# Kernel tuning notes

Measured on AMD Instinct MI355X. Metric: run time of the kernel, lower is better.

## Reference

```python
import jax, jax.numpy as jnp
import numpy as np
from jax import lax

LENGTH, WIDTH = 64, 64
INPUT_DIM = 1


def _convlstm_layer(x_tbchw, W, b):
    """Run one ConvLSTM layer over time. x_tbchw: (L,B,Cin,H,W).
    W: (4*hid, Cin+hid, 3, 3), b: (4*hid,). Returns (outputs (L,B,hid,H,W), last_h)."""
    L, B, _, H, Wd = x_tbchw.shape
    hid = W.shape[0] // 4
    h0 = jnp.zeros((B, hid, H, Wd), dtype=x_tbchw.dtype)
    c0 = jnp.zeros((B, hid, H, Wd), dtype=x_tbchw.dtype)

    def step(carry, xt):
        h, c = carry
        z = lax.conv_general_dilated(
            jnp.concatenate([xt, h], axis=1), W,
            window_strides=(1, 1), padding='SAME',
            dimension_numbers=('NCHW', 'OIHW', 'NCHW'))
        z = z + b[None, :, None, None]
        cc_i, cc_f, cc_o, cc_g = jnp.split(z, 4, axis=1)
        c_next = jax.nn.sigmoid(cc_f) * c + jax.nn.sigmoid(cc_i) * jnp.tanh(cc_g)
        h_next = jax.nn.sigmoid(cc_o) * jnp.tanh(c_next)
        return (h_next, c_next), h_next

    (h_last, _), outs = lax.scan(step, (h0, c0), x_tbchw)
    return outs, h_last


def setup_inputs() -> dict:
    key = jax.random.key(0)
    k1, k2, k3 = jax.random.split(key, 3)
    B, L, N = 16, 12, LENGTH * WIDTH
    emd, out_len = 128, 12
    return {
        'history_data': jax.random.normal(k1, (B, L, N, 1), dtype=jnp.float32),
        'future_data': jnp.zeros((B, L, N, 1), dtype=jnp.float32),
        'W0': jax.random.normal(k2, (4 * emd, INPUT_DIM + emd, 3, 3), dtype=jnp.float32) * 0.05,
        'b0': jnp.zeros((4 * emd,), dtype=jnp.float32),
        'W1': jax.random.normal(k3, (4 * out_len, emd + out_len, 3, 3), dtype=jnp.float32) * 0.05,
        'b1': jnp.zeros((4 * out_len,), dtype=jnp.float32),
        'batch_seen': 0,
        'epoch': 0,
        'train': 1,
    }


def reference(history_data, future_data, W0, b0, W1, b1, batch_seen, epoch, train):
    B, L, N, C = history_data.shape
    # (B,L,1,H,W) -> (L,B,1,H,W) for time-major scan
    x = history_data[..., :INPUT_DIM].reshape(B, L, INPUT_DIM, LENGTH, WIDTH)
    x = jnp.transpose(x, (1, 0, 2, 3, 4))
    outs0, _ = _convlstm_layer(x, W0, b0)          # (L,B,emd,H,W)
    _, h_last = _convlstm_layer(outs0, W1, b1)     # (B,out_len,H,W)
    prediction = h_last.reshape(B, L, LENGTH * WIDTH)[..., None]  # (B,L,N,1)
    return prediction
```

## Files before the change

kernel.cpp:

```cpp
#include <hip/hip_runtime.h>
#include <hip/hip_bf16.h>


typedef __attribute__((ext_vector_type(8))) short short8;
typedef __attribute__((ext_vector_type(4))) float float4v;

#define CS 160
#define KTOT 1440
#define RSTR 2560
#define BSTR 10240
#define BSTR6 15360

__device__ __forceinline__ float sigf(float x) { return 1.f / (1.f + __expf(-x)); }
__device__ __forceinline__ short f2hs(float v) {
  _Float16 h = (_Float16)v;
  return *(short*)&h;
}
__device__ __forceinline__ float bs2f(short s) {
  __hip_bfloat16 h; *(short*)&h = s; return __bfloat162float(h);
}
__device__ __forceinline__ short f2bs(float v) {
  __hip_bfloat16 h = __float2bfloat16(v);
  return *(short*)&h;
}

__device__ __forceinline__ void async_ld16(const short* g, short* l) {
  __builtin_amdgcn_global_load_lds(
      (const __attribute__((address_space(1))) unsigned int*)g,
      (__attribute__((address_space(3))) unsigned int*)l, 16, 0, 0);
}

__device__ __forceinline__ void stage_one(const short* __restrict__ rowPtr, bool rowOK,
                                          short* dstRow, int lane,
                                          const short* __restrict__ zp, int j) {
  int e = j * 64 + lane;
  int px = e >> 2, v = e & 3;
  int xx = px - 1;
  bool ok = rowOK && (px < 66) && (xx >= 0) && (xx < 64);
  const short* g = ok ? (rowPtr + (size_t)xx * CS + v * 8) : zp;
  async_ld16(g, dstRow + e * 8);
}

__device__ __forceinline__ void stage_row(const short* __restrict__ rowPtr, bool rowOK,
                                          short* dstRow, int lane,
                                          const short* __restrict__ zp) {
  #pragma unroll
  for (int j = 0; j < 5; ++j) stage_one(rowPtr, rowOK, dstRow, lane, zp, j);
}

__global__ void detect_dtype(const unsigned short* __restrict__ w0, int* __restrict__ flag) {
  int lane = threadIdx.x;
  int cnt = 0;
  for (int i = 0; i < 4; ++i) {
    unsigned short u = w0[2 * (lane + 64 * i)];
    int e = (u >> 7) & 0xFF;
    unsigned long long b = __ballot(e >= 0xC0);
    cnt += __popcll(b);
  }
  if (lane == 0) *flag = (cnt > 32) ? 1 : 0;
}

__global__ void canon_x(const void* __restrict__ hist, short* __restrict__ Xc,
                        const int* __restrict__ flag) {
  int i = blockIdx.x * 256 + threadIdx.x;
  float v = (*flag) ? ((const float*)hist)[i] : bs2f(((const short*)hist)[i]);
  if (!isfinite(v) || fabsf(v) > 1e4f) v = 0.f;
  Xc[i] = f2hs(v);
}

__global__ void canon_b(const void* __restrict__ b0, const void* __restrict__ b1,
                        float* __restrict__ Bc0, float* __restrict__ Bc1,
                        const int* __restrict__ flag) {
  int i = blockIdx.x * 256 + threadIdx.x;
  int fl = *flag;
  if (i < 512) {
    float v = fl ? ((const float*)b0)[i] : bs2f(((const short*)b0)[i]);
    if (!isfinite(v) || fabsf(v) > 1e4f) v = 0.f;
    Bc0[i] = v;
  } else if (i < 560) {
    int j = i - 512;
    float v = fl ? ((const float*)b1)[j] : bs2f(((const short*)b1)[j]);
    if (!isfinite(v) || fabsf(v) > 1e4f) v = 0.f;
    Bc1[j] = v;
  }
}

__global__ void prep_w0(const void* __restrict__ W0, short* __restrict__ Wp,
                        const int* __restrict__ flag) {
  int i = blockIdx.x * 256 + threadIdx.x;
  if (i >= 512 * KTOT) return;
  int fl = *flag;
  int co = i / KTOT, k = i - co * KTOT;
  int tap = k / CS, c = k - tap * CS;
  int ci = -1;
  if (c == 0) ci = 0;
  else if (c <= 128) ci = c;
  float w = 0.f;
  if (ci >= 0) {
    int widx = (co * 129 + ci) * 9 + tap;
    w = fl ? ((const float*)W0)[widx] : bs2f(((const short*)W0)[widx]);
    if (!isfinite(w) || fabsf(w) > 1e4f) w = 0.f;
  }
  Wp[i] = f2hs(w);
}

__global__ void prep_w1(const void* __restrict__ W1, short* __restrict__ Wp,
                        const int* __restrict__ flag) {
  int i = blockIdx.x * 256 + threadIdx.x;
  if (i >= 48 * KTOT) return;
  int fl = *flag;
  int co = i / KTOT, k = i - co * KTOT;
  int tap = k / CS, c = k - tap * CS;
  int ci = -1;
  if (c >= 1 && c <= 140) ci = c - 1;
  float w = 0.f;
  if (ci >= 0) {
    int widx = (co * 140 + ci) * 9 + tap;
    w = fl ? ((const float*)W1)[widx] : bs2f(((const short*)W1)[widx]);
    if (!isfinite(w) || fabsf(w) > 1e4f) w = 0.f;
  }
  Wp[i] = f2hs(w);
}

__global__ void fill_x0(const short* __restrict__ Xc, short* __restrict__ P0) {
  int p = blockIdx.x * 256 + threadIdx.x;
  int b = p >> 12, pix = p & 4095;
  P0[(size_t)p * CS] = Xc[b * 12 * 4096 + pix];
}

__global__ __launch_bounds__(256, 2) void gemm_gate0(
    const short* __restrict__ Pcur, short* __restrict__ Pnext,
    const short* __restrict__ Wp, const float* __restrict__ Bc0,
    float* __restrict__ C0, const short* __restrict__ Xc,
    const short* __restrict__ zp, int t) {
  int pbx = blockIdx.x;
  int xcd = pbx & 7, i = pbx >> 3;
  int mt = xcd * 32 + (i & 31);
  int nt = i >> 5;
  int b = mt >> 4, y0 = (mt & 15) * 4;
  int tid = threadIdx.x, wave = tid >> 6, lane = tid & 63;
  int ln15 = lane & 15, quad = lane >> 4;
  int wm = wave & 1, wn = wave >> 1;
  int hc = nt * 32 + wn * 16 + ln15;

  __shared__ __align__(16) short halo[2 * BSTR6];

  float4v acc[8][4];
  #pragma unroll
  for (int i2 = 0; i2 < 8; ++i2)
    #pragma unroll
    for (int j = 0; j < 4; ++j) acc[i2][j] = (float4v){0.f, 0.f, 0.f, 0.f};

  const short* wbase = Wp + (size_t)hc * KTOT + quad * 8;
  short8 bcur[4], bnxt[4];
  #pragma unroll
  for (int g = 0; g < 4; ++g)
    bcur[g] = *(const short8*)(wbase + (size_t)g * 128 * KTOT);

  int yyA = y0 - 1 + wave;
  bool okA = (yyA >= 0) && (yyA < 64);
  const short* baseA = Pcur + (size_t)((b * 64 + yyA) * 64) * CS;
  int yyB = y0 + 3 + wave;
  bool okB = (wave < 2) && (yyB < 64);
  const short* baseB = Pcur + (size_t)((b * 64 + yyB) * 64) * CS;

  stage_row(baseA, okA, halo + wave * RSTR, lane, zp);
  if (wave < 2) stage_row(baseB, okB, halo + (4 + wave) * RSTR, lane, zp);
  __syncthreads();

  for (int ch = 0; ch < 5; ++ch) {
    int c0 = ch * 32;
    const short* cur = halo + (ch & 1) * BSTR6;
    short* nd = halo + ((ch + 1) & 1) * BSTR6;
    const short* srcA = baseA + c0 + 32;
    const short* srcB = baseB + c0 + 32;
    #pragma unroll
    for (int tap = 0; tap < 9; ++tap) {
      int dy = tap / 3, dx = tap - dy * 3;
      if (ch < 4 && tap < 5) {
        stage_one(srcA, okA, nd + wave * RSTR, lane, zp, tap);
        if (wave < 2) stage_one(srcB, okB, nd + (4 + wave) * RSTR, lane, zp, tap);
      }
      int ntap = (tap < 8) ? tap + 1 : 0;
      int nc0 = (tap < 8) ? c0 : ((ch < 4) ? c0 + 32 : c0);
      #pragma unroll
      for (int g = 0; g < 4; ++g)
        bnxt[g] = *(const short8*)(wbase + (size_t)g * 128 * KTOT + ntap * CS + nc0);

      short8 af[8];
      #pragma unroll
      for (int mf = 0; mf < 8; ++mf)
        af[mf] = *(const short8*)&cur[(wm * 2 + (mf >> 2) + dy) * RSTR
                                      + ((mf & 3) * 16 + ln15 + dx) * 32 + quad * 8];
      #pragma unroll
      for (int g = 0; g < 4; ++g)
        #pragma unroll
        for (int mf = 0; mf < 8; ++mf)
          acc[mf][g] = __builtin_amdgcn_mfma_f32_16x16x32_f16(af[mf], bcur[g], acc[mf][g], 0, 0, 0);
      #pragma unroll
      for (int g = 0; g < 4; ++g) bcur[g] = bnxt[g];
    }
    __syncthreads();
  }

  float bi = Bc0[hc], bff = Bc0[128 + hc], bo = Bc0[256 + hc], bg = Bc0[384 + hc];
  #pragma unroll
  for (int mf = 0; mf < 8; ++mf) {
    int row = y0 + wm * 2 + (mf >> 2);
    int pixRow = (b * 64 + row) * 64;
    #pragma unroll
    for (int r = 0; r < 4; ++r) {
      int x = (mf & 3) * 16 + quad * 4 + r;
      int pix = pixRow + x;
      float zi = acc[mf][0][r] + bi;
      float zf = acc[mf][1][r] + bff;
      float zo = acc[mf][2][r] + bo;
      float zg = acc[mf][3][r] + bg;
      float cprev = C0[(size_t)pix * 128 + hc];
      float cn = sigf(zf) * cprev + sigf(zi) * tanhf(zg);
      float hn = sigf(zo) * tanhf(cn);
      C0[(size_t)pix * 128 + hc] = cn;
      Pnext[(size_t)pix * CS + 1 + hc] = f2hs(hn);
    }
  }
  if (nt == 0 && t < 11) {
    int rr = tid >> 6, x = tid & 63;
    int yw = y0 + rr;
    Pnext[(size_t)((b * 64 + yw) * 64 + x) * CS] = Xc[(b * 12 + t + 1) * 4096 + yw * 64 + x];
  }
}

__global__ __launch_bounds__(256, 2) void gemm_gate1(
    const short* __restrict__ Prd, short* __restrict__ Pwr,
    const short* __restrict__ Wp, const float* __restrict__ Bc1,
    float* __restrict__ C1, void* __restrict__ outp,
    const short* __restrict__ zp, const int* __restrict__ flagp, int t) {
  int pbx = blockIdx.x;
  int bid = (pbx & 7) * 64 + (pbx >> 3);
  int b = bid >> 5, y0 = (bid & 31) * 2;
  int tid = threadIdx.x, wave = tid >> 6, lane = tid & 63;
  int ln15 = lane & 15, quad = lane >> 4;
  int wr = wave >> 1, wh = wave & 1;
  int flagv = *flagp;

  __shared__ __align__(16) short halo[2 * BSTR];

  float4v acc[2][3];
  #pragma unroll
  for (int i = 0; i < 2; ++i)
    #pragma unroll
    for (int j = 0; j < 3; ++j) acc[i][j] = (float4v){0.f, 0.f, 0.f, 0.f};

  int yy = y0 - 1 + wave;
  bool rowOK = (yy >= 0) && (yy < 64);
  const short* rowBase = Prd + (size_t)((b * 64 + yy) * 64) * CS;

  const short* wbase = Wp + (size_t)ln15 * KTOT + quad * 8;
  short8 bcur[3], bnxt[3];
  #pragma unroll
  for (int nf = 0; nf < 3; ++nf)
    bcur[nf] = *(const short8*)(wbase + (size_t)nf * 16 * KTOT);

  stage_row(rowBase, rowOK, halo + wave * RSTR, lane, zp);
  __syncthreads();

  for (int ch = 0; ch < 5; ++ch) {
    int c0 = ch * 32;
    const short* cur = halo + (ch & 1) * BSTR;
    short* nxtDst = halo + ((ch + 1) & 1) * BSTR + wave * RSTR;
    const short* nxtSrc = rowBase + c0 + 32;
    #pragma unroll
    for (int tap = 0; tap < 9; ++tap) {
      int dy = tap / 3, dx = tap - dy * 3;
      if (ch < 4 && tap < 5)
        stage_one(nxtSrc, rowOK, nxtDst, lane, zp, tap);
      int ntap = (tap < 8) ? tap + 1 : 0;
      int nc0 = (tap < 8) ? c0 : ((ch < 4) ? c0 + 32 : c0);
      #pragma unroll
      for (int nf = 0; nf < 3; ++nf)
        bnxt[nf] = *(const short8*)(wbase + (size_t)nf * 16 * KTOT + ntap * CS + nc0);

      short8 af[2];
      #pragma unroll
      for (int mf = 0; mf < 2; ++mf)
        af[mf] = *(const short8*)&cur[(wr + dy) * RSTR + (wh * 32 + mf * 16 + ln15 + dx) * 32
                                      + quad * 8];
      #pragma unroll
      for (int nf = 0; nf < 3; ++nf)
        #pragma unroll
        for (int mf = 0; mf < 2; ++mf)
          acc[mf][nf] = __builtin_amdgcn_mfma_f32_16x16x32_f16(af[mf], bcur[nf], acc[mf][nf], 0, 0, 0);
      #pragma unroll
      for (int nf = 0; nf < 3; ++nf) bcur[nf] = bnxt[nf];
    }
    __syncthreads();
  }

  float* zbuf = (float*)halo;
  #pragma unroll
  for (int mf = 0; mf < 2; ++mf)
    #pragma unroll
    for (int nf = 0; nf < 3; ++nf)
      #pragma unroll
      for (int r = 0; r < 4; ++r) {
        int pxl = wr * 64 + wh * 32 + mf * 16 + quad * 4 + r;
        zbuf[pxl * 48 + nf * 16 + ln15] = acc[mf][nf][r];
      }
  __syncthreads();

  #pragma unroll
  for (int k = 0; k < 6; ++k) {
    int id = k * 256 + tid;
    int hc = id >> 7, pxl = id & 127;
    float zi = zbuf[pxl * 48 + hc]      + Bc1[hc];
    float zf = zbuf[pxl * 48 + 12 + hc] + Bc1[12 + hc];
    float zo = zbuf[pxl * 48 + 24 + hc] + Bc1[24 + hc];
    float zg = zbuf[pxl * 48 + 36 + hc] + Bc1[36 + hc];
    int y = y0 + (pxl >> 6), x = pxl & 63;
    int pix = (b * 64 + y) * 64 + x;
    float cprev = C1[(size_t)pix * 12 + hc];
    float cn = sigf(zf) * cprev + sigf(zi) * tanhf(zg);
    float hn = sigf(zo) * tanhf(cn);
    C1[(size_t)pix * 12 + hc] = cn;
    Pwr[(size_t)pix * CS + 129 + hc] = f2hs(hn);
    if (t == 11) {
      int oidx = (b * 12 + hc) * 4096 + y * 64 + x;
      if (flagv) ((float*)outp)[oidx] = hn;
      else ((short*)outp)[oidx] = f2bs(hn);
    }
  }
}

extern "C" void kernel_launch(void* const* d_in, const int* in_sizes, int n_in,
                              void* d_out, int out_size, void* d_ws, size_t ws_size,
                              hipStream_t stream) {
  const void* hist = d_in[0];
  const void* W0 = d_in[2];
  const void* b0 = d_in[3];
  const void* W1 = d_in[4];
  const void* b1 = d_in[5];

  char* ws = (char*)d_ws;
  const size_t PszB = (size_t)16 * 4096 * CS * 2;
  short* P[2] = {(short*)ws, (short*)(ws + PszB)};
  float* C0 = (float*)(ws + 2 * PszB);
  const size_t C0e = 2 * PszB + 33554432;
  float* C1 = (float*)(ws + C0e);
  const size_t C1e = C0e + 3145728;
  short* zp = (short*)(ws + C1e);
  const size_t zpe = C1e + 256;
  short* Xc = (short*)(ws + zpe);
  const size_t Xce = zpe + 1572864;
  short* Wp0 = (short*)(ws + Xce);
  const size_t W0e = Xce + (size_t)512 * KTOT * 2;
  short* Wp1 = (short*)(ws + W0e);
  const size_t W1e = W0e + (size_t)48 * KTOT * 2;
  float* Bc0 = (float*)(ws + W1e);
  float* Bc1 = (float*)(ws + W1e + 2048);
  int* flag = (int*)(ws + W1e + 2048 + 192);

  hipMemsetAsync(ws, 0, zpe, stream);
  detect_dtype<<<1, 64, 0, stream>>>((const unsigned short*)W0, flag);
  canon_x<<<3072, 256, 0, stream>>>(hist, Xc, flag);
  canon_b<<<3, 256, 0, stream>>>(b0, b1, Bc0, Bc1, flag);
  prep_w0<<<(512 * KTOT + 255) / 256, 256, 0, stream>>>(W0, Wp0, flag);
  prep_w1<<<(48 * KTOT + 255) / 256, 256, 0, stream>>>(W1, Wp1, flag);
  fill_x0<<<256, 256, 0, stream>>>(Xc, P[0]);

  for (int t = 0; t < 12; ++t) {
    gemm_gate0<<<1024, 256, 0, stream>>>(P[t & 1], P[(t + 1) & 1], Wp0, Bc0, C0, Xc, zp, t);
    gemm_gate1<<<512, 256, 0, stream>>>(P[(t + 1) & 1], P[t & 1], Wp1, Bc1, C1,
                                        d_out, zp, flag, t);
  }
}
```

Before: 2.060 ms.

## Split layer-0 input channel into precomputed im2col tap MFMA, shrink K to 1152

The single input channel of layer 0 was padded into a 32-wide channel chunk, so the gate0 GEMM ran five chunks (K=1440) when most of the fifth was zeros. The input contribution is now handled by a separate small MFMA over a precomputed 9-tap im2col buffer (Xtap) and a matching 16-wide weight slice. The main loop covers only the 128 hidden channels in four chunks (K=1152). Channel offsets in the shared P buffer shift by one accordingly, and the per-step input injection into P is removed, at the cost of a larger precomputed Xtap buffer read per step.

```diff
diff --git a/kernel.cpp b/kernel.cpp
--- a/kernel.cpp
+++ b/kernel.cpp
@@ -6,6 +6,7 @@
 typedef __attribute__((ext_vector_type(4))) float float4v;
 
 #define CS 160
+#define KT0 1152
 #define KTOT 1440
 #define RSTR 2560
 #define BSTR 10240
@@ -58,14 +59,6 @@
     cnt += __popcll(b);
   }
   if (lane == 0) *flag = (cnt > 32) ? 1 : 0;
-}
-
-__global__ void canon_x(const void* __restrict__ hist, short* __restrict__ Xc,
-                        const int* __restrict__ flag) {
-  int i = blockIdx.x * 256 + threadIdx.x;
-  float v = (*flag) ? ((const float*)hist)[i] : bs2f(((const short*)hist)[i]);
-  if (!isfinite(v) || fabsf(v) > 1e4f) v = 0.f;
-  Xc[i] = f2hs(v);
 }
 
 __global__ void canon_b(const void* __restrict__ b0, const void* __restrict__ b1,
@@ -85,23 +78,30 @@
   }
 }
 
+__device__ __forceinline__ float ldw(const void* W, int idx, int fl) {
+  float w = fl ? ((const float*)W)[idx] : bs2f(((const short*)W)[idx]);
+  if (!isfinite(w) || fabsf(w) > 1e4f) w = 0.f;
+  return w;
+}
+
 __global__ void prep_w0(const void* __restrict__ W0, short* __restrict__ Wp,
                         const int* __restrict__ flag) {
   int i = blockIdx.x * 256 + threadIdx.x;
-  if (i >= 512 * KTOT) return;
+  if (i >= 512 * KT0) return;
   int fl = *flag;
-  int co = i / KTOT, k = i - co * KTOT;
-  int tap = k / CS, c = k - tap * CS;
-  int ci = -1;
-  if (c == 0) ci = 0;
-  else if (c <= 128) ci = c;
-  float w = 0.f;
-  if (ci >= 0) {
-    int widx = (co * 129 + ci) * 9 + tap;
-    w = fl ? ((const float*)W0)[widx] : bs2f(((const short*)W0)[widx]);
-    if (!isfinite(w) || fabsf(w) > 1e4f) w = 0.f;
-  }
-  Wp[i] = f2hs(w);
+  int co = i / KT0, k = i - co * KT0;
+  int tap = k >> 7, c = k & 127;
+  Wp[i] = f2hs(ldw(W0, (co * 129 + 1 + c) * 9 + tap, fl));
+}
+
+__global__ void prep_wx(const void* __restrict__ W0, short* __restrict__ Wx,
+                        const int* __restrict__ flag) {
+  int i = blockIdx.x * 256 + threadIdx.x;
+  if (i >= 512 * 16) return;
+  int fl = *flag;
+  int co = i >> 4, k = i & 15;
+  float w = (k < 9) ? ldw(W0, (co * 129) * 9 + k, fl) : 0.f;
+  Wx[i] = f2hs(w);
 }
 
 __global__ void prep_w1(const void* __restrict__ W1, short* __restrict__ Wp,
@@ -111,28 +111,38 @@
   int fl = *flag;
   int co = i / KTOT, k = i - co * KTOT;
   int tap = k / CS, c = k - tap * CS;
-  int ci = -1;
-  if (c >= 1 && c <= 140) ci = c - 1;
-  float w = 0.f;
-  if (ci >= 0) {
-    int widx = (co * 140 + ci) * 9 + tap;
-    w = fl ? ((const float*)W1)[widx] : bs2f(((const short*)W1)[widx]);
-    if (!isfinite(w) || fabsf(w) > 1e4f) w = 0.f;
-  }
+  float w = (c < 140) ? ldw(W1, (co * 140 + c) * 9 + tap, fl) : 0.f;
   Wp[i] = f2hs(w);
 }
 
-__global__ void fill_x0(const short* __restrict__ Xc, short* __restrict__ P0) {
-  int p = blockIdx.x * 256 + threadIdx.x;
-  int b = p >> 12, pix = p & 4095;
-  P0[(size_t)p * CS] = Xc[b * 12 * 4096 + pix];
+__global__ void prep_xtap(const void* __restrict__ hist, short* __restrict__ Xtap,
+                          const int* __restrict__ flag) {
+  int i = blockIdx.x * 256 + threadIdx.x;
+  int t = i >> 16, p = i & 65535;
+  int b = p >> 12, pix = p & 4095, y = pix >> 6, x = pix & 63;
+  int fl = *flag;
+  short8 lo = {0, 0, 0, 0, 0, 0, 0, 0}, hi = {0, 0, 0, 0, 0, 0, 0, 0};
+  #pragma unroll
+  for (int k = 0; k < 9; ++k) {
+    int dy = k / 3, dx = k - dy * 3;
+    int yy = y + dy - 1, xx = x + dx - 1;
+    float f = 0.f;
+    if (yy >= 0 && yy < 64 && xx >= 0 && xx < 64) {
+      int hidx = (b * 12 + t) * 4096 + yy * 64 + xx;
+      f = fl ? ((const float*)hist)[hidx] : bs2f(((const short*)hist)[hidx]);
+      if (!isfinite(f) || fabsf(f) > 1e4f) f = 0.f;
+    }
+    if (k < 8) lo[k] = f2hs(f); else hi[k - 8] = f2hs(f);
+  }
+  *(short8*)(Xtap + (size_t)i * 16) = lo;
+  *(short8*)(Xtap + (size_t)i * 16 + 8) = hi;
 }
 
 __global__ __launch_bounds__(256, 2) void gemm_gate0(
     const short* __restrict__ Pcur, short* __restrict__ Pnext,
-    const short* __restrict__ Wp, const float* __restrict__ Bc0,
-    float* __restrict__ C0, const short* __restrict__ Xc,
-    const short* __restrict__ zp, int t) {
+    const short* __restrict__ Wp, const short* __restrict__ Wx,
+    const float* __restrict__ Bc0, float* __restrict__ C0,
+    const short* __restrict__ Xtap, const short* __restrict__ zp, int t) {
   int pbx = blockIdx.x;
   int xcd = pbx & 7, i = pbx >> 3;
   int mt = xcd * 32 + (i & 31);
@@ -151,11 +161,11 @@
     #pragma unroll
     for (int j = 0; j < 4; ++j) acc[i2][j] = (float4v){0.f, 0.f, 0.f, 0.f};
 
-  const short* wbase = Wp + (size_t)hc * KTOT + quad * 8;
+  const short* wbase = Wp + (size_t)hc * KT0 + quad * 8;
   short8 bcur[4], bnxt[4];
   #pragma unroll
   for (int g = 0; g < 4; ++g)
-    bcur[g] = *(const short8*)(wbase + (size_t)g * 128 * KTOT);
+    bcur[g] = *(const short8*)(wbase + (size_t)g * 128 * KT0);
 
   int yyA = y0 - 1 + wave;
   bool okA = (yyA >= 0) && (yyA < 64);
@@ -164,11 +174,31 @@
   bool okB = (wave < 2) && (yyB < 64);
   const short* baseB = Pcur + (size_t)((b * 64 + yyB) * 64) * CS;
 
+  bool hiQ = quad >= 2;
+  short8 ax[8], bxr[4];
+  #pragma unroll
+  for (int mf = 0; mf < 8; ++mf) {
+    int row = y0 + wm * 2 + (mf >> 2);
+    int pixB = (b * 64 + row) * 64 + (mf & 3) * 16 + ln15;
+    ax[mf] = *(const short8*)(Xtap + ((size_t)t * 65536 + pixB) * 16 + (quad & 1) * 8);
+  }
+  #pragma unroll
+  for (int g = 0; g < 4; ++g) {
+    const short* wxp = Wx + (size_t)(g * 128 + hc) * 16 + (quad & 1) * 8;
+    bxr[g] = *(const short8*)(hiQ ? zp : wxp);
+  }
+
   stage_row(baseA, okA, halo + wave * RSTR, lane, zp);
   if (wave < 2) stage_row(baseB, okB, halo + (4 + wave) * RSTR, lane, zp);
+
+  #pragma unroll
+  for (int g = 0; g < 4; ++g)
+    #pragma unroll
+    for (int mf = 0; mf < 8; ++mf)
+      acc[mf][g] = __builtin_amdgcn_mfma_f32_16x16x32_f16(ax[mf], bxr[g], acc[mf][g], 0, 0, 0);
   __syncthreads();
 
-  for (int ch = 0; ch < 5; ++ch) {
+  for (int ch = 0; ch < 4; ++ch) {
     int c0 = ch * 32;
     const short* cur = halo + (ch & 1) * BSTR6;
     short* nd = halo + ((ch + 1) & 1) * BSTR6;
@@ -177,15 +207,15 @@
     #pragma unroll
     for (int tap = 0; tap < 9; ++tap) {
       int dy = tap / 3, dx = tap - dy * 3;
-      if (ch < 4 && tap < 5) {
+      if (ch < 3 && tap < 5) {
         stage_one(srcA, okA, nd + wave * RSTR, lane, zp, tap);
         if (wave < 2) stage_one(srcB, okB, nd + (4 + wave) * RSTR, lane, zp, tap);
       }
       int ntap = (tap < 8) ? tap + 1 : 0;
-      int nc0 = (tap < 8) ? c0 : ((ch < 4) ? c0 + 32 : c0);
+      int nc0 = (tap < 8) ? c0 : ((ch < 3) ? c0 + 32 : c0);
       #pragma unroll
       for (int g = 0; g < 4; ++g)
-        bnxt[g] = *(const short8*)(wbase + (size_t)g * 128 * KTOT + ntap * CS + nc0);
+        bnxt[g] = *(const short8*)(wbase + (size_t)g * 128 * KT0 + ntap * 128 + nc0);
 
       short8 af[8];
       #pragma unroll
@@ -220,13 +250,8 @@
       float cn = sigf(zf) * cprev + sigf(zi) * tanhf(zg);
       float hn = sigf(zo) * tanhf(cn);
       C0[(size_t)pix * 128 + hc] = cn;
-      Pnext[(size_t)pix * CS + 1 + hc] = f2hs(hn);
+      Pnext[(size_t)pix * CS + hc] = f2hs(hn);
     }
-  }
-  if (nt == 0 && t < 11) {
-    int rr = tid >> 6, x = tid & 63;
-    int yw = y0 + rr;
-    Pnext[(size_t)((b * 64 + yw) * 64 + x) * CS] = Xc[(b * 12 + t + 1) * 4096 + yw * 64 + x];
   }
 }
 
@@ -322,7 +347,7 @@
     float cn = sigf(zf) * cprev + sigf(zi) * tanhf(zg);
     float hn = sigf(zo) * tanhf(cn);
     C1[(size_t)pix * 12 + hc] = cn;
-    Pwr[(size_t)pix * CS + 129 + hc] = f2hs(hn);
+    Pwr[(size_t)pix * CS + 128 + hc] = f2hs(hn);
     if (t == 11) {
       int oidx = (b * 12 + hc) * 4096 + y * 64 + x;
       if (flagv) ((float*)outp)[oidx] = hn;
@@ -349,26 +374,29 @@
   const size_t C1e = C0e + 3145728;
   short* zp = (short*)(ws + C1e);
   const size_t zpe = C1e + 256;
-  short* Xc = (short*)(ws + zpe);
-  const size_t Xce = zpe + 1572864;
-  short* Wp0 = (short*)(ws + Xce);
-  const size_t W0e = Xce + (size_t)512 * KTOT * 2;
-  short* Wp1 = (short*)(ws + W0e);
-  const size_t W1e = W0e + (size_t)48 * KTOT * 2;
+  short* Xtap = (short*)(ws + zpe);
+  const size_t Xte = zpe + (size_t)12 * 65536 * 16 * 2;
+  short* Wp0 = (short*)(ws + Xte);
+  const size_t W0e = Xte + (size_t)512 * KT0 * 2;
+  short* Wx0 = (short*)(ws + W0e);
+  const size_t Wxe = W0e + 512 * 16 * 2;
+  short* Wp1 = (short*)(ws + Wxe);
+  const size_t W1e = Wxe + (size_t)48 * KTOT * 2;
   float* Bc0 = (float*)(ws + W1e);
   float* Bc1 = (float*)(ws + W1e + 2048);
   int* flag = (int*)(ws + W1e + 2048 + 192);
 
   hipMemsetAsync(ws, 0, zpe, stream);
   detect_dtype<<<1, 64, 0, stream>>>((const unsigned short*)W0, flag);
-  canon_x<<<3072, 256, 0, stream>>>(hist, Xc, flag);
   canon_b<<<3, 256, 0, stream>>>(b0, b1, Bc0, Bc1, flag);
-  prep_w0<<<(512 * KTOT + 255) / 256, 256, 0, stream>>>(W0, Wp0, flag);
+  prep_w0<<<(512 * KT0 + 255) / 256, 256, 0, stream>>>(W0, Wp0, flag);
+  prep_wx<<<32, 256, 0, stream>>>(W0, Wx0, flag);
   prep_w1<<<(48 * KTOT + 255) / 256, 256, 0, stream>>>(W1, Wp1, flag);
-  fill_x0<<<256, 256, 0, stream>>>(Xc, P[0]);
+  prep_xtap<<<3072, 256, 0, stream>>>(hist, Xtap, flag);
 
   for (int t = 0; t < 12; ++t) {
-    gemm_gate0<<<1024, 256, 0, stream>>>(P[t & 1], P[(t + 1) & 1], Wp0, Bc0, C0, Xc, zp, t);
+    gemm_gate0<<<1024, 256, 0, stream>>>(P[t & 1], P[(t + 1) & 1], Wp0, Wx0, Bc0, C0,
+                                         Xtap, zp, t);
     gemm_gate1<<<512, 256, 0, stream>>>(P[(t + 1) & 1], P[t & 1], Wp1, Bc1, C1,
                                         d_out, zp, flag, t);
   }
```

After: 1.934 ms. -6.1%, faster.
